# Kernel tuning notes

Measured on AMD Instinct MI355X. Metric: run time of the kernel, lower is better.

Reference implementation:

```python
import jax, jax.numpy as jnp
import numpy as np

B, N, D = 2, 2048, 768
H = 12
HD = D // H  # 64

def setup_inputs() -> dict:
    key = jax.random.key(0)
    ks = jax.random.split(key, 5)
    scale = 1.0 / np.sqrt(D)
    return {
        "x": jax.random.normal(ks[0], (B, N, D), dtype=jnp.float32),
        "W_kqv": jax.random.normal(ks[1], (H, 3 * HD, D), dtype=jnp.float32) * scale,
        "b_kqv": jax.random.normal(ks[2], (H, 3 * HD), dtype=jnp.float32) * 0.01,
        "W_proj": jax.random.normal(ks[3], (D, D), dtype=jnp.float32) * scale,
        "b_proj": jax.random.normal(ks[4], (D,), dtype=jnp.float32) * 0.01,
    }

def reference(x, W_kqv, b_kqv, W_proj, b_proj):
    # Per-head Linear: x @ W_h^T + b_h, all heads at once -> [B, H, N, 3*HD]
    kqv = jnp.einsum('bnd,hod->bhno', x, W_kqv) + b_kqv[None, :, None, :]
    k, q, v = jnp.split(kqv, 3, axis=-1)  # each [B, H, N, HD]
    # scores = q @ k^T / sqrt(head_dim)  (attention_scores(a=k, b=q))
    scores = jnp.einsum('bhqd,bhkd->bhqk', q, k) / jnp.sqrt(jnp.asarray(HD, x.dtype))
    # causal mask (tril): masked_fill with -inf where mask == 0
    causal = jnp.tril(jnp.ones((N, N), dtype=bool))
    scores = jnp.where(causal[None, None, :, :], scores, -jnp.inf)
    attn = jax.nn.softmax(scores, axis=-1)
    sa = jnp.einsum('bhqk,bhkd->bhqd', attn, v)  # [B, H, N, HD]
    # concat heads along feature dim (head order preserved)
    sa = sa.transpose(0, 2, 1, 3).reshape(B, N, D)
    # output projection
    return sa @ W_proj.T + b_proj
```

## Files before the change

### kernel.cpp

```cpp
#include <hip/hip_runtime.h>

#define BB 2
#define SEQ 2048
#define DIM 768
#define NH 12
#define HD 64

typedef _Float16 half8 __attribute__((ext_vector_type(8)));
typedef float floatx4 __attribute__((ext_vector_type(4)));

__device__ __forceinline__ void gl_lds16(const _Float16* g, _Float16* l) {
    __builtin_amdgcn_global_load_lds(
        (const __attribute__((address_space(1))) void*)g,
        (__attribute__((address_space(3))) void*)l, 16, 0, 0);
}

__global__ __launch_bounds__(256)
void cvt3(const float* __restrict__ s0, _Float16* __restrict__ d0, int nb0,
          const float* __restrict__ s1, _Float16* __restrict__ d1, int nb1,
          const float* __restrict__ s2, _Float16* __restrict__ d2) {
    int b = blockIdx.x;
    const float* s; _Float16* d;
    if (b < nb0)            { s = s0; d = d0; }
    else if (b < nb0 + nb1) { s = s1; d = d1; b -= nb0; }
    else                    { s = s2; d = d2; b -= nb0 + nb1; }
    const int i = (b * 256 + threadIdx.x) * 8;
    float4 a = *(const float4*)(s + i);
    float4 c = *(const float4*)(s + i + 4);
    half8 h;
    h[0] = (_Float16)a.x; h[1] = (_Float16)a.y; h[2] = (_Float16)a.z; h[3] = (_Float16)a.w;
    h[4] = (_Float16)c.x; h[5] = (_Float16)c.y; h[6] = (_Float16)c.z; h[7] = (_Float16)c.w;
    *(half8*)(d + i) = h;
}

#define GEMM_CORE(APTR, BPTR)                                                   \
    __shared__ _Float16 Asl[2][128 * 32];                                       \
    __shared__ _Float16 Bsl[2][128 * 32];                                       \
    const int t = threadIdx.x, w = t >> 6, lane = t & 63;                       \
    const int quad = lane >> 4, l15 = lane & 15;                                \
    const int wm = w >> 1, wn = w & 1;                                          \
    const int m0 = blockIdx.y * 128, c0 = blockIdx.x * 128;                     \
    const floatx4 z4 = {0.f, 0.f, 0.f, 0.f};                                    \
    floatx4 acc[4][4];                                                          \
    _Pragma("unroll") for (int i = 0; i < 4; ++i)                               \
        _Pragma("unroll") for (int j = 0; j < 4; ++j) acc[i][j] = z4;           \
    const _Float16* pA = APTR + (size_t)(m0 + w * 32 + l15) * DIM + quad * 8;   \
    const _Float16* pB = BPTR + (size_t)(c0 + w * 32 + l15) * DIM + quad * 8;   \
    gl_lds16(pA,            &Asl[0][(w * 2 + 0) * 512]);                        \
    gl_lds16(pA + 16 * DIM, &Asl[0][(w * 2 + 1) * 512]);                        \
    gl_lds16(pB,            &Bsl[0][(w * 2 + 0) * 512]);                        \
    gl_lds16(pB + 16 * DIM, &Bsl[0][(w * 2 + 1) * 512]);                        \
    for (int k0 = 0, it = 0; k0 < DIM; k0 += 32, ++it) {                        \
        const int buf = it & 1;                                                 \
        __syncthreads();                                                        \
        if (k0 + 32 < DIM) {                                                    \
            gl_lds16(pA + k0 + 32,            &Asl[buf ^ 1][(w * 2 + 0) * 512]);\
            gl_lds16(pA + k0 + 32 + 16 * DIM, &Asl[buf ^ 1][(w * 2 + 1) * 512]);\
            gl_lds16(pB + k0 + 32,            &Bsl[buf ^ 1][(w * 2 + 0) * 512]);\
            gl_lds16(pB + k0 + 32 + 16 * DIM, &Bsl[buf ^ 1][(w * 2 + 1) * 512]);\
        }                                                                       \
        half8 af[4], bf[4];                                                     \
        _Pragma("unroll") for (int i = 0; i < 4; ++i)                           \
            af[i] = *(const half8*)&Asl[buf][(wm * 4 + i) * 512 + lane * 8];    \
        _Pragma("unroll") for (int j = 0; j < 4; ++j)                           \
            bf[j] = *(const half8*)&Bsl[buf][(wn * 4 + j) * 512 + lane * 8];    \
        _Pragma("unroll") for (int i = 0; i < 4; ++i)                           \
            _Pragma("unroll") for (int j = 0; j < 4; ++j)                       \
                acc[i][j] = __builtin_amdgcn_mfma_f32_16x16x32_f16(             \
                    af[i], bf[j], acc[i][j], 0, 0, 0);                          \
    }

__global__ __launch_bounds__(256)
void kqv_gemm2(const _Float16* __restrict__ xh, const _Float16* __restrict__ Wh,
               const float* __restrict__ bias, _Float16* __restrict__ kb,
               _Float16* __restrict__ qb, _Float16* __restrict__ vb) {
    GEMM_CORE(xh, Wh)
    #pragma unroll
    for (int j = 0; j < 4; ++j) {
        const int cbase = c0 + (wn * 4 + j) * 16;
        const int h = cbase / 192;
        const int rem = cbase - h * 192;
        const int part = rem >> 6;
        const int d = (rem & 63) + l15;
        _Float16* dst = (part == 0) ? kb : (part == 1 ? qb : vb);
        const float bv = bias[cbase + l15];
        #pragma unroll
        for (int i = 0; i < 4; ++i)
            #pragma unroll
            for (int r = 0; r < 4; ++r) {
                const int m = m0 + (wm * 4 + i) * 16 + quad * 4 + r;
                const int bidx = m >> 11, n = m & (SEQ - 1);
                dst[(((size_t)(bidx * NH + h) * SEQ + n) << 6) + d] =
                    (_Float16)(acc[i][j][r] + bv);
            }
    }
}

__global__ __launch_bounds__(256)
void proj_gemm2(const _Float16* __restrict__ A, const _Float16* __restrict__ Wh,
                const float* __restrict__ bias, float* __restrict__ out) {
    GEMM_CORE(A, Wh)
    #pragma unroll
    for (int j = 0; j < 4; ++j) {
        const int cbase = c0 + (wn * 4 + j) * 16;
        const float bv = bias[cbase + l15];
        #pragma unroll
        for (int i = 0; i < 4; ++i)
            #pragma unroll
            for (int r = 0; r < 4; ++r) {
                const int m = m0 + (wm * 4 + i) * 16 + quad * 4 + r;
                out[(size_t)m * DIM + cbase + l15] = acc[i][j][r] + bv;
            }
    }
}

__global__ __launch_bounds__(256)
void v_transpose(const _Float16* __restrict__ vb, _Float16* __restrict__ vbT) {
    __shared__ _Float16 T[64 * 72];
    const int t = threadIdx.x;
    const int s0 = blockIdx.x * 64;
    const size_t base = (size_t)blockIdx.y * (SEQ * HD);
    {
        const int s = t >> 2, doff = (t & 3) * 16;
        const _Float16* src = vb + base + (size_t)(s0 + s) * HD + doff;
        *(half8*)&T[s * 72 + doff]     = *(const half8*)src;
        *(half8*)&T[s * 72 + doff + 8] = *(const half8*)(src + 8);
    }
    __syncthreads();
    {
        const int d = t >> 2, soff = (t & 3) * 16;
        half8 o0, o1;
        #pragma unroll
        for (int k = 0; k < 8; ++k) o0[k] = T[(soff + k) * 72 + d];
        #pragma unroll
        for (int k = 0; k < 8; ++k) o1[k] = T[(soff + 8 + k) * 72 + d];
        _Float16* dst = vbT + base + (size_t)d * SEQ + s0 + soff;
        *(half8*)dst       = o0;
        *(half8*)(dst + 8) = o1;
    }
}

__global__ __launch_bounds__(256)
void attn_mfma(const _Float16* __restrict__ qb, const _Float16* __restrict__ kbuf,
               const _Float16* __restrict__ vbT, _Float16* __restrict__ sa) {
    __shared__ _Float16 Kl[2][64 * 64];
    __shared__ _Float16 Vl[2][64 * 64];
    __shared__ _Float16 Pl[4][2][16 * 72];
    const int Q = 15 - blockIdx.x;
    const int bh = blockIdx.y;
    const int t = threadIdx.x, w = t >> 6, lane = t & 63, quad = lane >> 4, l15 = lane & 15;
    const size_t base = (size_t)bh * (SEQ * HD);
    const int i0 = Q * 128 + w * 32;
    const _Float16* Kg = kbuf + base;
    const _Float16* Vg = vbT + base;
    const int nkt = 2 * Q + 2;

    const int lr = lane >> 3, gg = lane & 7;
    const int gs = (gg ^ (lr & 7)) * 8;

    half8 aq[2][2];
    #pragma unroll
    for (int rt = 0; rt < 2; ++rt)
        #pragma unroll
        for (int ks = 0; ks < 2; ++ks) {
            aq[rt][ks] = *(const half8*)(qb + base +
                          (size_t)(i0 + rt * 16 + l15) * HD + ks * 32 + quad * 8);
            #pragma unroll
            for (int k = 0; k < 8; ++k)
                aq[rt][ks][k] = aq[rt][ks][k] * (_Float16)0.125f;
        }

    const floatx4 z4 = {0.f, 0.f, 0.f, 0.f};
    floatx4 O[2][4];
    float l_part[2][4];
    #pragma unroll
    for (int rt = 0; rt < 2; ++rt)
        #pragma unroll
        for (int k = 0; k < 4; ++k) { O[rt][k] = z4; l_part[rt][k] = 0.f; }

    #pragma unroll
    for (int p = 0; p < 2; ++p) {
        const int c = w * 2 + p, row = c * 8 + lr;
        gl_lds16(Kg + (size_t)row * HD + gs,  &Kl[0][c * 512]);
        gl_lds16(Vg + (size_t)row * SEQ + gs, &Vl[0][c * 512]);
    }

    const int swz = l15 & 7;

    for (int kt = 0; kt < nkt; ++kt) {
        const int buf = kt & 1;
        const int j0 = kt * 64;
        __syncthreads();

        if (kt + 1 < nkt) {
            const _Float16* Kn = Kg + (size_t)(j0 + 64) * HD;
            const _Float16* Vn = Vg + (j0 + 64);
            #pragma unroll
            for (int p = 0; p < 2; ++p) {
                const int c = w * 2 + p, row = c * 8 + lr;
                gl_lds16(Kn + (size_t)row * HD + gs,  &Kl[buf ^ 1][c * 512]);
                gl_lds16(Vn + (size_t)row * SEQ + gs, &Vl[buf ^ 1][c * 512]);
            }
        }
        if (j0 > i0 + 31) continue;

        floatx4 S[2][4];
        #pragma unroll
        for (int rt = 0; rt < 2; ++rt)
            #pragma unroll
            for (int nt = 0; nt < 4; ++nt) S[rt][nt] = z4;
        #pragma unroll
        for (int ks = 0; ks < 2; ++ks)
            #pragma unroll
            for (int nt = 0; nt < 4; ++nt) {
                half8 bk = *(const half8*)&Kl[buf][(nt * 16 + l15) * 64 +
                                                   (((ks * 4 + quad) ^ swz) << 3)];
                S[0][nt] = __builtin_amdgcn_mfma_f32_16x16x32_f16(aq[0][ks], bk, S[0][nt], 0, 0, 0);
                S[1][nt] = __builtin_amdgcn_mfma_f32_16x16x32_f16(aq[1][ks], bk, S[1][nt], 0, 0, 0);
            }

        const bool needmask = (j0 + 63 > i0);
        asm volatile("" ::: "memory");
        #pragma unroll
        for (int rt = 0; rt < 2; ++rt)
            #pragma unroll
            for (int nt = 0; nt < 4; ++nt) {
                const int j = j0 + nt * 16 + l15;
                #pragma unroll
                for (int r = 0; r < 4; ++r) {
                    float p = __expf(S[rt][nt][r]);
                    if (needmask && j > (i0 + rt * 16 + quad * 4 + r)) p = 0.f;
                    l_part[rt][r] += p;
                    Pl[w][rt][(quad * 4 + r) * 72 + nt * 16 + l15] = (_Float16)p;
                }
            }
        asm volatile("" ::: "memory");
        #pragma unroll
        for (int ks = 0; ks < 2; ++ks) {
            half8 ap0 = *(const half8*)&Pl[w][0][l15 * 72 + ks * 32 + quad * 8];
            half8 ap1 = *(const half8*)&Pl[w][1][l15 * 72 + ks * 32 + quad * 8];
            #pragma unroll
            for (int dt = 0; dt < 4; ++dt) {
                half8 bv = *(const half8*)&Vl[buf][(dt * 16 + l15) * 64 +
                                                    (((ks * 4 + quad) ^ swz) << 3)];
                O[0][dt] = __builtin_amdgcn_mfma_f32_16x16x32_f16(ap0, bv, O[0][dt], 0, 0, 0);
                O[1][dt] = __builtin_amdgcn_mfma_f32_16x16x32_f16(ap1, bv, O[1][dt], 0, 0, 0);
            }
        }
    }

    const int bidx = bh / NH, h = bh - bidx * NH;
    #pragma unroll
    for (int rt = 0; rt < 2; ++rt)
        #pragma unroll
        for (int r = 0; r < 4; ++r) {
            float rs = l_part[rt][r];
            #pragma unroll
            for (int off = 1; off < 16; off <<= 1) rs += __shfl_xor(rs, off);
            const float inv = 1.0f / rs;
            const int i = i0 + rt * 16 + quad * 4 + r;
            #pragma unroll
            for (int dt = 0; dt < 4; ++dt)
                sa[(size_t)(bidx * SEQ + i) * DIM + h * HD + dt * 16 + l15] =
                    (_Float16)(O[rt][dt][r] * inv);
        }
}

extern "C" void kernel_launch(void* const* d_in, const int* in_sizes, int n_in,
                              void* d_out, int out_size, void* d_ws, size_t ws_size,
                              hipStream_t stream) {
    (void)in_sizes; (void)n_in; (void)out_size; (void)ws_size;
    const float* x  = (const float*)d_in[0];
    const float* Wk = (const float*)d_in[1];
    const float* bk = (const float*)d_in[2];
    const float* Wp = (const float*)d_in[3];
    const float* bp = (const float*)d_in[4];
    float* out = (float*)d_out;

    _Float16* ws = (_Float16*)d_ws;
    const size_t per = (size_t)BB * NH * SEQ * HD;
    const int nx = BB * SEQ * DIM;
    const int nwk = NH * 3 * HD * DIM;
    _Float16* kb  = ws;
    _Float16* qb  = ws + per;
    _Float16* vb  = ws + 2 * per;
    _Float16* vbT = ws + 3 * per;
    _Float16* sa  = ws + 4 * per;
    _Float16* xh  = ws + 5 * per;
    _Float16* Wkh = xh + nx;
    _Float16* Wph = Wkh + nwk;

    const int nb0 = nx / 2048, nb1 = nwk / 2048, nb2 = (DIM * DIM) / 2048;
    cvt3<<<dim3(nb0 + nb1 + nb2), 256, 0, stream>>>(x, xh, nb0, Wk, Wkh, nb1, Wp, Wph);

    kqv_gemm2 <<<dim3(18, 32), 256, 0, stream>>>(xh, Wkh, bk, kb, qb, vb);
    v_transpose<<<dim3(32, 24), 256, 0, stream>>>(vb, vbT);
    attn_mfma <<<dim3(16, 24), 256, 0, stream>>>(qb, kb, vbT, sa);
    proj_gemm2<<<dim3(6, 32), 256, 0, stream>>>(sa, Wph, bp, out);
}
```

Baseline: 215.2 us.

## Split causal attention across KV chunks with combine kernel and retile projection GEMM

Attention query tiles with long KV ranges are split into up to four 8-tile KV chunks (40 blocks per head instead of 16), with partial O and row sums written to workspace and merged by a new combine kernel. This balances causal work and fills more CUs. Softmax now uses exp2 with a log2e-folded Q scale, separate masked and unmasked paths, and an XOR-swizzled P buffer to cut LDS bank conflicts. The output projection switches to a 128x64 tile GEMM with twice as many blocks. The costs are an extra launch, partial-result traffic, and fp16 rounding of the unnormalized partial O sums.

```diff
diff --git a/kernel.cpp b/kernel.cpp
--- a/kernel.cpp
+++ b/kernel.cpp
@@ -97,12 +97,50 @@
 }
 
 __global__ __launch_bounds__(256)
-void proj_gemm2(const _Float16* __restrict__ A, const _Float16* __restrict__ Wh,
+void proj_gemm3(const _Float16* __restrict__ A, const _Float16* __restrict__ Wh,
                 const float* __restrict__ bias, float* __restrict__ out) {
-    GEMM_CORE(A, Wh)
-    #pragma unroll
-    for (int j = 0; j < 4; ++j) {
-        const int cbase = c0 + (wn * 4 + j) * 16;
+    __shared__ _Float16 Asl[2][128 * 32];
+    __shared__ _Float16 Bsl[2][64 * 32];
+    const int t = threadIdx.x, w = t >> 6, lane = t & 63;
+    const int quad = lane >> 4, l15 = lane & 15;
+    const int wm = w >> 1, wn = w & 1;
+    const int m0 = blockIdx.y * 128, c0 = blockIdx.x * 64;
+    const floatx4 z4 = {0.f, 0.f, 0.f, 0.f};
+    floatx4 acc[4][2];
+    #pragma unroll
+    for (int i = 0; i < 4; ++i)
+        #pragma unroll
+        for (int j = 0; j < 2; ++j) acc[i][j] = z4;
+    const _Float16* pA = A  + (size_t)(m0 + w * 32 + l15) * DIM + quad * 8;
+    const _Float16* pB = Wh + (size_t)(c0 + w * 16 + l15) * DIM + quad * 8;
+    gl_lds16(pA,            &Asl[0][(w * 2 + 0) * 512]);
+    gl_lds16(pA + 16 * DIM, &Asl[0][(w * 2 + 1) * 512]);
+    gl_lds16(pB,            &Bsl[0][w * 512]);
+    for (int k0 = 0, it = 0; k0 < DIM; k0 += 32, ++it) {
+        const int buf = it & 1;
+        __syncthreads();
+        if (k0 + 32 < DIM) {
+            gl_lds16(pA + k0 + 32,            &Asl[buf ^ 1][(w * 2 + 0) * 512]);
+            gl_lds16(pA + k0 + 32 + 16 * DIM, &Asl[buf ^ 1][(w * 2 + 1) * 512]);
+            gl_lds16(pB + k0 + 32,            &Bsl[buf ^ 1][w * 512]);
+        }
+        half8 af[4], bf[2];
+        #pragma unroll
+        for (int i = 0; i < 4; ++i)
+            af[i] = *(const half8*)&Asl[buf][(wm * 4 + i) * 512 + lane * 8];
+        #pragma unroll
+        for (int j = 0; j < 2; ++j)
+            bf[j] = *(const half8*)&Bsl[buf][(wn * 2 + j) * 512 + lane * 8];
+        #pragma unroll
+        for (int i = 0; i < 4; ++i)
+            #pragma unroll
+            for (int j = 0; j < 2; ++j)
+                acc[i][j] = __builtin_amdgcn_mfma_f32_16x16x32_f16(
+                    af[i], bf[j], acc[i][j], 0, 0, 0);
+    }
+    #pragma unroll
+    for (int j = 0; j < 2; ++j) {
+        const int cbase = c0 + (wn * 2 + j) * 16;
         const float bv = bias[cbase + l15];
         #pragma unroll
         for (int i = 0; i < 4; ++i)
@@ -142,23 +180,32 @@
 
 __global__ __launch_bounds__(256)
 void attn_mfma(const _Float16* __restrict__ qb, const _Float16* __restrict__ kbuf,
-               const _Float16* __restrict__ vbT, _Float16* __restrict__ sa) {
+               const _Float16* __restrict__ vbT, _Float16* __restrict__ sa,
+               _Float16* __restrict__ Opart, float* __restrict__ lpart) {
     __shared__ _Float16 Kl[2][64 * 64];
     __shared__ _Float16 Vl[2][64 * 64];
-    __shared__ _Float16 Pl[4][2][16 * 72];
-    const int Q = 15 - blockIdx.x;
+    __shared__ _Float16 Pl[8][16 * 64];
+    int u = 39 - blockIdx.x, q, p, np;
+    if (u < 4)       { q = u;               p = 0;     np = 1; }
+    else if (u < 12) { int v = u - 4;  q = 4  + (v >> 1); p = v & 1; np = 2; }
+    else if (u < 24) { int v = u - 12; q = 8  + v / 3;    p = v % 3; np = 3; }
+    else             { int v = u - 24; q = 12 + (v >> 2); p = v & 3; np = 4; }
+    const int ntiles = 2 * q + 2;
+    const int kt0 = p * 8;
+    const int ktn = (p == np - 1) ? (ntiles - kt0) : 8;
+
     const int bh = blockIdx.y;
     const int t = threadIdx.x, w = t >> 6, lane = t & 63, quad = lane >> 4, l15 = lane & 15;
     const size_t base = (size_t)bh * (SEQ * HD);
-    const int i0 = Q * 128 + w * 32;
+    const int i0 = q * 128 + w * 32;
     const _Float16* Kg = kbuf + base;
     const _Float16* Vg = vbT + base;
-    const int nkt = 2 * Q + 2;
 
     const int lr = lane >> 3, gg = lane & 7;
     const int gs = (gg ^ (lr & 7)) * 8;
 
     half8 aq[2][2];
+    const _Float16 qs = (_Float16)(0.125f * 1.44269504f);
     #pragma unroll
     for (int rt = 0; rt < 2; ++rt)
         #pragma unroll
@@ -166,8 +213,7 @@
             aq[rt][ks] = *(const half8*)(qb + base +
                           (size_t)(i0 + rt * 16 + l15) * HD + ks * 32 + quad * 8);
             #pragma unroll
-            for (int k = 0; k < 8; ++k)
-                aq[rt][ks][k] = aq[rt][ks][k] * (_Float16)0.125f;
+            for (int k = 0; k < 8; ++k) aq[rt][ks][k] *= qs;
         }
 
     const floatx4 z4 = {0.f, 0.f, 0.f, 0.f};
@@ -179,25 +225,27 @@
         for (int k = 0; k < 4; ++k) { O[rt][k] = z4; l_part[rt][k] = 0.f; }
 
     #pragma unroll
-    for (int p = 0; p < 2; ++p) {
-        const int c = w * 2 + p, row = c * 8 + lr;
-        gl_lds16(Kg + (size_t)row * HD + gs,  &Kl[0][c * 512]);
-        gl_lds16(Vg + (size_t)row * SEQ + gs, &Vl[0][c * 512]);
+    for (int pp = 0; pp < 2; ++pp) {
+        const int c = w * 2 + pp, row = c * 8 + lr;
+        gl_lds16(Kg + (size_t)(kt0 * 64 + row) * HD + gs,  &Kl[0][c * 512]);
+        gl_lds16(Vg + (size_t)row * SEQ + kt0 * 64 + gs,   &Vl[0][c * 512]);
     }
 
     const int swz = l15 & 7;
-
-    for (int kt = 0; kt < nkt; ++kt) {
-        const int buf = kt & 1;
+    const int prow = quad * 4;
+
+    for (int it = 0; it < ktn; ++it) {
+        const int kt = kt0 + it;
+        const int buf = it & 1;
         const int j0 = kt * 64;
         __syncthreads();
 
-        if (kt + 1 < nkt) {
+        if (it + 1 < ktn) {
             const _Float16* Kn = Kg + (size_t)(j0 + 64) * HD;
             const _Float16* Vn = Vg + (j0 + 64);
             #pragma unroll
-            for (int p = 0; p < 2; ++p) {
-                const int c = w * 2 + p, row = c * 8 + lr;
+            for (int pp = 0; pp < 2; ++pp) {
+                const int c = w * 2 + pp, row = c * 8 + lr;
                 gl_lds16(Kn + (size_t)row * HD + gs,  &Kl[buf ^ 1][c * 512]);
                 gl_lds16(Vn + (size_t)row * SEQ + gs, &Vl[buf ^ 1][c * 512]);
             }
@@ -219,26 +267,42 @@
                 S[1][nt] = __builtin_amdgcn_mfma_f32_16x16x32_f16(aq[1][ks], bk, S[1][nt], 0, 0, 0);
             }
 
-        const bool needmask = (j0 + 63 > i0);
         asm volatile("" ::: "memory");
-        #pragma unroll
-        for (int rt = 0; rt < 2; ++rt)
-            #pragma unroll
-            for (int nt = 0; nt < 4; ++nt) {
-                const int j = j0 + nt * 16 + l15;
-                #pragma unroll
-                for (int r = 0; r < 4; ++r) {
-                    float p = __expf(S[rt][nt][r]);
-                    if (needmask && j > (i0 + rt * 16 + quad * 4 + r)) p = 0.f;
-                    l_part[rt][r] += p;
-                    Pl[w][rt][(quad * 4 + r) * 72 + nt * 16 + l15] = (_Float16)p;
+        if (j0 + 63 > i0) {
+            #pragma unroll
+            for (int rt = 0; rt < 2; ++rt)
+                #pragma unroll
+                for (int nt = 0; nt < 4; ++nt) {
+                    const int j = j0 + nt * 16 + l15;
+                    #pragma unroll
+                    for (int r = 0; r < 4; ++r) {
+                        float pv = exp2f(S[rt][nt][r]);
+                        if (j > (i0 + rt * 16 + prow + r)) pv = 0.f;
+                        l_part[rt][r] += pv;
+                        const int row = prow + r, col = nt * 16 + l15;
+                        Pl[w * 2 + rt][row * 64 + (((col >> 3) ^ (row & 7)) << 3) + (col & 7)] =
+                            (_Float16)pv;
+                    }
                 }
-            }
+        } else {
+            #pragma unroll
+            for (int rt = 0; rt < 2; ++rt)
+                #pragma unroll
+                for (int nt = 0; nt < 4; ++nt)
+                    #pragma unroll
+                    for (int r = 0; r < 4; ++r) {
+                        float pv = exp2f(S[rt][nt][r]);
+                        l_part[rt][r] += pv;
+                        const int row = prow + r, col = nt * 16 + l15;
+                        Pl[w * 2 + rt][row * 64 + (((col >> 3) ^ (row & 7)) << 3) + (col & 7)] =
+                            (_Float16)pv;
+                    }
+        }
         asm volatile("" ::: "memory");
         #pragma unroll
         for (int ks = 0; ks < 2; ++ks) {
-            half8 ap0 = *(const half8*)&Pl[w][0][l15 * 72 + ks * 32 + quad * 8];
-            half8 ap1 = *(const half8*)&Pl[w][1][l15 * 72 + ks * 32 + quad * 8];
+            half8 ap0 = *(const half8*)&Pl[w * 2 + 0][l15 * 64 + (((ks * 4 + quad) ^ swz) << 3)];
+            half8 ap1 = *(const half8*)&Pl[w * 2 + 1][l15 * 64 + (((ks * 4 + quad) ^ swz) << 3)];
             #pragma unroll
             for (int dt = 0; dt < 4; ++dt) {
                 half8 bv = *(const half8*)&Vl[buf][(dt * 16 + l15) * 64 +
@@ -249,21 +313,77 @@
         }
     }
 
+    if (np == 1) {
+        const int bidx = bh / NH, h = bh - bidx * NH;
+        #pragma unroll
+        for (int rt = 0; rt < 2; ++rt)
+            #pragma unroll
+            for (int r = 0; r < 4; ++r) {
+                float rs = l_part[rt][r];
+                #pragma unroll
+                for (int off = 1; off < 16; off <<= 1) rs += __shfl_xor(rs, off);
+                const float inv = 1.0f / rs;
+                const int i = i0 + rt * 16 + quad * 4 + r;
+                #pragma unroll
+                for (int dt = 0; dt < 4; ++dt)
+                    sa[(size_t)(bidx * SEQ + i) * DIM + h * HD + dt * 16 + l15] =
+                        (_Float16)(O[rt][dt][r] * inv);
+            }
+    } else {
+        const size_t slot = ((size_t)(bh * 16 + q) * 4 + p);
+        _Float16* Od = Opart + slot * 8192;
+        float*    ld = lpart + slot * 128;
+        #pragma unroll
+        for (int rt = 0; rt < 2; ++rt)
+            #pragma unroll
+            for (int r = 0; r < 4; ++r) {
+                float rs = l_part[rt][r];
+                #pragma unroll
+                for (int off = 1; off < 16; off <<= 1) rs += __shfl_xor(rs, off);
+                const int row = w * 32 + rt * 16 + quad * 4 + r;
+                ld[row] = rs;
+                #pragma unroll
+                for (int dt = 0; dt < 4; ++dt)
+                    Od[row * 64 + dt * 16 + l15] = (_Float16)O[rt][dt][r];
+            }
+    }
+}
+
+__global__ __launch_bounds__(256)
+void attn_combine(const _Float16* __restrict__ Opart, const float* __restrict__ lpart,
+                  _Float16* __restrict__ sa) {
+    const int q = 4 + blockIdx.x;
+    const int bh = blockIdx.y;
+    const int np = (q < 8) ? 2 : (q < 12 ? 3 : 4);
+    const int t = threadIdx.x;
+    const int row = t >> 1, d0 = (t & 1) * 32;
+    const size_t slot0 = (size_t)(bh * 16 + q) * 4;
+
+    float lsum = 0.f;
+    for (int p = 0; p < np; ++p) lsum += lpart[(slot0 + p) * 128 + row];
+
+    float acc[32];
+    #pragma unroll
+    for (int k = 0; k < 32; ++k) acc[k] = 0.f;
+    for (int p = 0; p < np; ++p) {
+        const _Float16* src = Opart + (slot0 + p) * 8192 + row * 64 + d0;
+        #pragma unroll
+        for (int v = 0; v < 4; ++v) {
+            half8 a = *(const half8*)(src + v * 8);
+            #pragma unroll
+            for (int k = 0; k < 8; ++k) acc[v * 8 + k] += (float)a[k];
+        }
+    }
+    const float inv = 1.0f / lsum;
     const int bidx = bh / NH, h = bh - bidx * NH;
-    #pragma unroll
-    for (int rt = 0; rt < 2; ++rt)
-        #pragma unroll
-        for (int r = 0; r < 4; ++r) {
-            float rs = l_part[rt][r];
-            #pragma unroll
-            for (int off = 1; off < 16; off <<= 1) rs += __shfl_xor(rs, off);
-            const float inv = 1.0f / rs;
-            const int i = i0 + rt * 16 + quad * 4 + r;
-            #pragma unroll
-            for (int dt = 0; dt < 4; ++dt)
-                sa[(size_t)(bidx * SEQ + i) * DIM + h * HD + dt * 16 + l15] =
-                    (_Float16)(O[rt][dt][r] * inv);
-        }
+    _Float16* dst = sa + (size_t)(bidx * SEQ + q * 128 + row) * DIM + h * HD + d0;
+    #pragma unroll
+    for (int v = 0; v < 4; ++v) {
+        half8 o;
+        #pragma unroll
+        for (int k = 0; k < 8; ++k) o[k] = (_Float16)(acc[v * 8 + k] * inv);
+        *(half8*)(dst + v * 8) = o;
+    }
 }
 
 extern "C" void kernel_launch(void* const* d_in, const int* in_sizes, int n_in,
@@ -281,6 +401,7 @@
     const size_t per = (size_t)BB * NH * SEQ * HD;
     const int nx = BB * SEQ * DIM;
     const int nwk = NH * 3 * HD * DIM;
+    const int nwp = DIM * DIM;
     _Float16* kb  = ws;
     _Float16* qb  = ws + per;
     _Float16* vb  = ws + 2 * per;
@@ -289,12 +410,15 @@
     _Float16* xh  = ws + 5 * per;
     _Float16* Wkh = xh + nx;
     _Float16* Wph = Wkh + nwk;
-
-    const int nb0 = nx / 2048, nb1 = nwk / 2048, nb2 = (DIM * DIM) / 2048;
+    _Float16* Opart = Wph + nwp;
+    float*    lpart = (float*)(Opart + (size_t)24 * 16 * 4 * 8192);
+
+    const int nb0 = nx / 2048, nb1 = nwk / 2048, nb2 = nwp / 2048;
     cvt3<<<dim3(nb0 + nb1 + nb2), 256, 0, stream>>>(x, xh, nb0, Wk, Wkh, nb1, Wp, Wph);
 
-    kqv_gemm2 <<<dim3(18, 32), 256, 0, stream>>>(xh, Wkh, bk, kb, qb, vb);
+    kqv_gemm2  <<<dim3(18, 32), 256, 0, stream>>>(xh, Wkh, bk, kb, qb, vb);
     v_transpose<<<dim3(32, 24), 256, 0, stream>>>(vb, vbT);
-    attn_mfma <<<dim3(16, 24), 256, 0, stream>>>(qb, kb, vbT, sa);
-    proj_gemm2<<<dim3(6, 32), 256, 0, stream>>>(sa, Wph, bp, out);
-}
+    attn_mfma  <<<dim3(40, 24), 256, 0, stream>>>(qb, kb, vbT, sa, Opart, lpart);
+    attn_combine<<<dim3(12, 24), 256, 0, stream>>>(Opart, lpart, sa);
+    proj_gemm3 <<<dim3(12, 32), 256, 0, stream>>>(sa, Wph, bp, out);
+}
```

Result: faster. 188.8 us (-12.3%).
